# Optimization experiments

Measured on AMD Instinct MI355X. Metric: run time of the kernel, lower is better.

## Reference

```python
import jax, jax.numpy as jnp
import numpy as np
import math

D_MODEL = 128
N_HEAD = 8
D_K = D_MODEL // N_HEAD
NEG_INF = -1e30


def setup_inputs() -> dict:
    key = jax.random.key(0)
    ks = jax.random.split(key, 8)
    B, N, D = 4, 2048, D_MODEL
    s = 1.0 / math.sqrt(D)
    x = jax.random.normal(ks[0], (B, D, N), dtype=jnp.float32)
    mask = jnp.ones((B, N), dtype=jnp.float32)
    Wq = jax.random.normal(ks[1], (D, D), dtype=jnp.float32) * s
    Wk = jax.random.normal(ks[2], (D, D), dtype=jnp.float32) * s
    Wv = jax.random.normal(ks[3], (D, D), dtype=jnp.float32) * s
    Wfc = jax.random.normal(ks[4], (D, D), dtype=jnp.float32) * s
    z = jnp.zeros((D,), dtype=jnp.float32)
    return {"x": x, "mask": mask, "Wq": Wq, "bq": z, "Wk": Wk, "bk": z,
            "Wv": Wv, "bv": z, "Wfc": Wfc, "bfc": z}


def reference(x, mask, Wq, bq, Wk, bk, Wv, bv, Wfc, bfc):
    # x: [B, D, N], mask: [B, N]
    B, D, N = x.shape
    xt = jnp.swapaxes(x, 1, 2)  # [B, N, D]
    q = (xt @ Wq.T + bq).reshape(B, N, N_HEAD, D_K)
    k = (xt @ Wk.T + bk).reshape(B, N, N_HEAD, D_K)
    v = (xt @ Wv.T + bv).reshape(B, N, N_HEAD, D_K)
    # scores: [B, H, Nq, Nk]; NOTE: original scales by sqrt(d_model), not sqrt(d_k)
    scores = jnp.einsum('bnhd,bmhd->bhnm', q, k) / jnp.sqrt(jnp.float32(D))
    # multiplicative mask_logits over the key dimension
    m = mask[:, None, None, :]  # [B, 1, 1, Nk]
    scores = scores * m + (1.0 - m) * NEG_INF
    atten = jax.nn.softmax(scores, axis=-1)  # dropout is identity (p=0 / eval)
    out = jnp.einsum('bhnm,bmhd->bnhd', atten, v).reshape(B, N, D)
    out = out @ Wfc.T + bfc
    return jnp.swapaxes(out, 1, 2)  # [B, D, N]
```

## Files before the change

### kernel.cpp

```cpp
#include <hip/hip_runtime.h>
#include <stdint.h>

#define BSZ  4
#define NSEQ 2048
#define DM   128
#define NH   8
#define DK   16
#define LOG2E 1.4426950408889634f
#define SCALE_QL 0.1275156338341935f
#define W_SCALE 3.814697265625e-6f

typedef __bf16          bf16x8v __attribute__((ext_vector_type(8)));
typedef float           f32x4   __attribute__((ext_vector_type(4)));
typedef float           f32x16  __attribute__((ext_vector_type(16)));
typedef unsigned short  u16x8   __attribute__((ext_vector_type(8)));
typedef unsigned short  u16x4   __attribute__((ext_vector_type(4)));
typedef unsigned int    u32x2   __attribute__((ext_vector_type(2)));
typedef unsigned int    u32x4   __attribute__((ext_vector_type(4)));

__device__ __forceinline__ unsigned short f2bf(float f) {
    unsigned u = __float_as_uint(f);
    u = (u + 0x7fffu + ((u >> 16) & 1u)) >> 16;
    return (unsigned short)u;
}

__device__ __forceinline__ unsigned int pack2bf(float a, float b) {
#if __has_builtin(__builtin_amdgcn_cvt_pk_bf16_f32)
    typedef __bf16 bf16x2 __attribute__((ext_vector_type(2)));
    bf16x2 v = __builtin_amdgcn_cvt_pk_bf16_f32(a, b);
    return __builtin_bit_cast(unsigned int, v);
#else
    return (unsigned)f2bf(a) | ((unsigned)f2bf(b) << 16);
#endif
}

__device__ __forceinline__ float exp2_(float x) {
#if __has_builtin(__builtin_amdgcn_exp2f)
    return __builtin_amdgcn_exp2f(x);
#else
    return exp2f(x);
#endif
}

__device__ __forceinline__ f32x4 mfma16(u16x8 a, u16x8 b, f32x4 c) {
    return __builtin_amdgcn_mfma_f32_16x16x32_bf16(
        __builtin_bit_cast(bf16x8v, a), __builtin_bit_cast(bf16x8v, b), c, 0, 0, 0);
}
__device__ __forceinline__ f32x16 mfma32(u16x8 a, u16x8 b, f32x16 c) {
    return __builtin_amdgcn_mfma_f32_32x32x16_bf16(
        __builtin_bit_cast(bf16x8v, a), __builtin_bit_cast(bf16x8v, b), c, 0, 0, 0);
}

__device__ __forceinline__ void build_bfrags(const f32x16& S, u16x8& bfe, u16x8& bfo) {
    const u32x4 f1 = {pack2bf(S[0],  S[1]),  pack2bf(S[2],  S[3]),
                      pack2bf(S[4],  S[5]),  pack2bf(S[6],  S[7])};
    const u32x4 f2 = {pack2bf(S[8],  S[9]),  pack2bf(S[10], S[11]),
                      pack2bf(S[12], S[13]), pack2bf(S[14], S[15])};
    bfe = __builtin_bit_cast(u16x8, f1);
    bfo = __builtin_bit_cast(u16x8, f2);
}

__global__ __launch_bounds__(256) void k_prep(
    const float* __restrict__ Wq, const float* __restrict__ Wk,
    const float* __restrict__ Wv, const float* __restrict__ Wfc,
    const float* __restrict__ mask,
    unsigned short* __restrict__ WqB, unsigned short* __restrict__ WkB,
    unsigned short* __restrict__ WvB, unsigned short* __restrict__ WfcB,
    unsigned short* __restrict__ VW2)
{
    const int gt = blockIdx.x * 256 + threadIdx.x;
    if (gt < DM * DM) {
        WqB[gt]  = f2bf(Wq[gt] * SCALE_QL);
        WkB[gt]  = f2bf(Wk[gt]);
        WvB[gt]  = f2bf(Wv[gt]);
        WfcB[gt] = f2bf(Wfc[gt]);
    } else if (gt < DM * DM + BSZ * NSEQ) {
        const int i  = gt - DM * DM;
        const int kv = i & (NSEQ - 1);
        const int bb = i >> 11;
        const unsigned short w16 = f2bf(mask[i] * W_SCALE);
        unsigned short* dst = VW2 +
            (((size_t)(bb * NH) * 128 + (kv >> 4)) << 9) +
            (16 + ((kv >> 2) & 1) * 32) * 8 + (kv & 3) + 4 * ((kv >> 3) & 1);
#pragma unroll
        for (int hh = 0; hh < NH; ++hh)
            dst[(size_t)hh * 128 * 512] = w16;
    }
}

__global__ __launch_bounds__(768) void k_qkv(
    const float* __restrict__ x,
    const unsigned short* __restrict__ WqB, const float* __restrict__ bq,
    const unsigned short* __restrict__ WkB, const float* __restrict__ bk,
    const unsigned short* __restrict__ WvB, const float* __restrict__ bv,
    const float* __restrict__ mask,
    unsigned short* __restrict__ Q, unsigned short* __restrict__ Kb,
    unsigned short* __restrict__ VW2)
{
    __shared__ __align__(16) float xs[DM * 36];
    const int tid = threadIdx.x;

    const int b  = blockIdx.x >> 6;
    const int n0 = (blockIdx.x & 63) << 5;

#pragma unroll
    for (int i = tid; i < 1024; i += 768) {
        const int d = i >> 3, c4 = (i & 7) << 2;
        *reinterpret_cast<f32x4*>(&xs[d * 36 + c4]) =
            *reinterpret_cast<const f32x4*>(x + (size_t)(b * DM + d) * NSEQ + n0 + c4);
    }
    __syncthreads();

    const int lane = tid & 63;
    const int wv   = tid >> 6;
    const int mat  = wv >> 2;
    const int nt   = (wv >> 1) & 1;
    const int th   = wv & 1;
    const int c    = lane & 15;
    const int quad = lane >> 4;
    const int col  = n0 + nt * 16 + c;

    u16x8 xf[4];
#pragma unroll
    for (int kk = 0; kk < 4; ++kk) {
        float f[8];
#pragma unroll
        for (int j = 0; j < 8; ++j)
            f[j] = xs[(kk * 32 + quad * 8 + j) * 36 + nt * 16 + c];
        u32x4 u = {pack2bf(f[0], f[1]), pack2bf(f[2], f[3]),
                   pack2bf(f[4], f[5]), pack2bf(f[6], f[7])};
        xf[kk] = __builtin_bit_cast(u16x8, u);
    }

    const unsigned short* W = (mat == 0) ? WqB : (mat == 1) ? WkB : WvB;
    const float* bias = (mat == 0) ? bq : (mat == 1) ? bk : bv;
    const float  sc   = (mat == 0) ? SCALE_QL : 1.0f;
    const float  vwsc = (mat == 2) ? mask[b * NSEQ + col] * W_SCALE : 0.f;
    const int    g    = col >> 4;
    const int    roff = ((col >> 2) & 1) * 32;
    const int    j7   = (col & 3) | (((col >> 3) & 1) << 2);

#pragma unroll
    for (int tt = 0; tt < 4; ++tt) {
        const int t = th * 4 + tt;
        f32x4 acc = {0.f, 0.f, 0.f, 0.f};
#pragma unroll
        for (int kk = 0; kk < 4; ++kk)
            acc = mfma16(*reinterpret_cast<const u16x8*>(
                             W + (t * 16 + c) * DM + kk * 32 + quad * 8),
                         xf[kk], acc);
        if (mat == 2) {
            unsigned short* vwp = VW2 +
                (((size_t)((b * NH + t) * 128 + g)) << 9) + j7;
#pragma unroll
            for (int r = 0; r < 4; ++r)
                vwp[(quad * 4 + r + roff) * 8] =
                    f2bf((acc[r] + bias[t * 16 + quad * 4 + r]) * vwsc);
        } else {
            u16x4 pk;
#pragma unroll
            for (int r = 0; r < 4; ++r)
                pk[r] = f2bf(acc[r] + bias[t * 16 + quad * 4 + r] * sc);
            *reinterpret_cast<u16x4*>(
                (mat == 0 ? Q : Kb) + ((size_t)(b * NH + t) * NSEQ + col) * DK +
                quad * 4) = pk;
        }
    }
}

__global__ __launch_bounds__(256, 4) void k_attn(
    const unsigned short* __restrict__ Q,
    const unsigned short* __restrict__ Kb,
    const unsigned short* __restrict__ VW2,
    unsigned short* __restrict__ AO)
{
    __shared__ __align__(16) float smem[256 + 2 * 4 * 32 * 20];
    const int tid  = threadIdx.x;
    const int lane = tid & 63;
    const int w    = tid >> 6;
    const int q32  = lane & 31;
    const int hi   = lane >> 5;

    const int bid = ((int)blockIdx.x & 7) * 128 + ((int)blockIdx.x >> 3);
    const int b  = bid >> 8;
    const int h  = (bid >> 5) & 7;
    const int n0 = (bid & 31) << 6;
    const int bh = b * NH + h;

    const u16x8 uqA = *reinterpret_cast<const u16x8*>(
        Q + ((size_t)bh * NSEQ + n0 + q32) * DK + 8 * hi);
    const u16x8 uqB = *reinterpret_cast<const u16x8*>(
        Q + ((size_t)bh * NSEQ + n0 + 32 + q32) * DK + 8 * hi);

    const unsigned short* Kp = Kb + (size_t)bh * NSEQ * DK + 8 * hi;
    const unsigned short* Ap = VW2 + (((size_t)bh * 128) << 9) + lane * 8;

    f32x16 accA = {};
    f32x16 accB = {};
    const f32x16 z16 = {};
    const int kvb = w * (NSEQ / 4);

    u16x8 nk0 = *reinterpret_cast<const u16x8*>(Kp + (size_t)(kvb + q32) * DK);
    u16x8 nk1 = *reinterpret_cast<const u16x8*>(Kp + (size_t)(kvb + 32 + q32) * DK);

#pragma unroll 1
    for (int it = 0; it < 8; ++it) {
        const int kv0 = kvb + it * 64;
        const int g0  = kv0 >> 4;
        const u16x8 va0 = *reinterpret_cast<const u16x8*>(Ap + ((size_t)(g0    ) << 9));
        const u16x8 va1 = *reinterpret_cast<const u16x8*>(Ap + ((size_t)(g0 + 1) << 9));
        const u16x8 va2 = *reinterpret_cast<const u16x8*>(Ap + ((size_t)(g0 + 2) << 9));
        const u16x8 va3 = *reinterpret_cast<const u16x8*>(Ap + ((size_t)(g0 + 3) << 9));

        {
            __builtin_amdgcn_s_setprio(1);
            f32x16 SA = mfma32(nk0, uqA, z16);
            f32x16 SB = mfma32(nk0, uqB, z16);
            __builtin_amdgcn_s_setprio(0);
            if (it < 7)
                nk0 = *reinterpret_cast<const u16x8*>(
                    Kp + (size_t)(kv0 + 64 + q32) * DK);
#pragma unroll
            for (int i = 0; i < 16; ++i) SA[i] = exp2_(SA[i]);
#pragma unroll
            for (int i = 0; i < 16; ++i) SB[i] = exp2_(SB[i]);
            u16x8 bfA1, bfA2, bfB1, bfB2;
            build_bfrags(SA, bfA1, bfA2);
            build_bfrags(SB, bfB1, bfB2);
            __builtin_amdgcn_s_setprio(1);
            accA = mfma32(va0, bfA1, accA);
            accB = mfma32(va0, bfB1, accB);
            accA = mfma32(va1, bfA2, accA);
            accB = mfma32(va1, bfB2, accB);
            __builtin_amdgcn_s_setprio(0);
        }

        {
            __builtin_amdgcn_s_setprio(1);
            f32x16 SA = mfma32(nk1, uqA, z16);
            f32x16 SB = mfma32(nk1, uqB, z16);
            __builtin_amdgcn_s_setprio(0);
            if (it < 7)
                nk1 = *reinterpret_cast<const u16x8*>(
                    Kp + (size_t)(kv0 + 96 + q32) * DK);
#pragma unroll
            for (int i = 0; i < 16; ++i) SA[i] = exp2_(SA[i]);
#pragma unroll
            for (int i = 0; i < 16; ++i) SB[i] = exp2_(SB[i]);
            u16x8 bfA1, bfA2, bfB1, bfB2;
            build_bfrags(SA, bfA1, bfA2);
            build_bfrags(SB, bfB1, bfB2);
            __builtin_amdgcn_s_setprio(1);
            accA = mfma32(va2, bfA1, accA);
            accB = mfma32(va2, bfB1, accB);
            accA = mfma32(va3, bfA2, accA);
            accB = mfma32(va3, bfB2, accB);
            __builtin_amdgcn_s_setprio(0);
        }
    }

    float* Lsm = smem;
    float* Osm = smem + 256;
    {
        float* Orow = Osm + w * 640 + q32 * 20;
        *reinterpret_cast<f32x4*>(Orow + (hi ? 4 : 0)) =
            f32x4{accA[0], accA[1], accA[2], accA[3]};
        *reinterpret_cast<f32x4*>(Orow + (hi ? 12 : 8)) =
            f32x4{accA[4], accA[5], accA[6], accA[7]};
        if (!hi) Lsm[w * 32 + q32] = accA[8];
        float* Orow2 = Orow + 2560;
        *reinterpret_cast<f32x4*>(Orow2 + (hi ? 4 : 0)) =
            f32x4{accB[0], accB[1], accB[2], accB[3]};
        *reinterpret_cast<f32x4*>(Orow2 + (hi ? 12 : 8)) =
            f32x4{accB[4], accB[5], accB[6], accB[7]};
        if (!hi) Lsm[128 + w * 32 + q32] = accB[8];
    }
    __syncthreads();

    const int q   = tid >> 3;
    const int dk2 = (tid & 7) * 2;
#pragma unroll
    for (int t2 = 0; t2 < 2; ++t2) {
        const float* Lt = Lsm + t2 * 128;
        const float l = Lt[q] + Lt[32 + q] + Lt[64 + q] + Lt[96 + q];
        const float* Oq = Osm + t2 * 2560 + q * 20 + dk2;
        const float v0 = Oq[0] + Oq[640] + Oq[1280] + Oq[1920];
        const float v1 = Oq[1] + Oq[641] + Oq[1281] + Oq[1921];
        const float inv = 1.0f / l;
        *reinterpret_cast<unsigned int*>(
            AO + ((size_t)(b * NSEQ) + n0 + t2 * 32 + q) * DM + h * DK + dk2) =
            pack2bf(v0 * inv, v1 * inv);
    }
}

__global__ __launch_bounds__(256) void k_fc(
    const unsigned short* __restrict__ AO,
    const unsigned short* __restrict__ WfcB, const float* __restrict__ bfc,
    float* __restrict__ out)
{
    const int lane = threadIdx.x & 63;
    const int w    = threadIdx.x >> 6;
    const int c    = lane & 15;
    const int quad = lane >> 4;
    const int b    = blockIdx.x >> 8;
    const int n0   = ((blockIdx.x >> 1) & 127) << 4;
    const int t    = (blockIdx.x & 1) * 4 + w;

    u16x8 af[4];
#pragma unroll
    for (int kk = 0; kk < 4; ++kk)
        af[kk] = *reinterpret_cast<const u16x8*>(
            AO + ((size_t)(b * NSEQ) + n0 + c) * DM + kk * 32 + quad * 8);

    f32x4 acc = {0.f, 0.f, 0.f, 0.f};
#pragma unroll
    for (int kk = 0; kk < 4; ++kk)
        acc = mfma16(*reinterpret_cast<const u16x8*>(
                         WfcB + (t * 16 + c) * DM + kk * 32 + quad * 8),
                     af[kk], acc);
#pragma unroll
    for (int r = 0; r < 4; ++r)
        out[(size_t)(b * DM + t * 16 + quad * 4 + r) * NSEQ + n0 + c] =
            acc[r] + bfc[t * 16 + quad * 4 + r];
}

extern "C" void kernel_launch(void* const* d_in, const int* in_sizes, int n_in,
                              void* d_out, int out_size, void* d_ws, size_t ws_size,
                              hipStream_t stream)
{
    const float* x    = (const float*)d_in[0];
    const float* mask = (const float*)d_in[1];
    const float* Wq   = (const float*)d_in[2];
    const float* bq   = (const float*)d_in[3];
    const float* Wk   = (const float*)d_in[4];
    const float* bk   = (const float*)d_in[5];
    const float* Wv   = (const float*)d_in[6];
    const float* bv   = (const float*)d_in[7];
    const float* Wfc  = (const float*)d_in[8];
    const float* bfc  = (const float*)d_in[9];
    float* out = (float*)d_out;

    const size_t QKV_ELEMS = (size_t)BSZ * NH * NSEQ * DK;
    unsigned short* Q    = (unsigned short*)d_ws;
    unsigned short* Kb   = Q + QKV_ELEMS;
    unsigned short* AO   = Kb + QKV_ELEMS;
    unsigned short* WfcB = AO + QKV_ELEMS;
    unsigned short* VW2  = WfcB + DM * DM;
    unsigned short* WqB  = VW2 + (size_t)BSZ * NH * 128 * 512;
    unsigned short* WkB  = WqB + DM * DM;
    unsigned short* WvB  = WkB + DM * DM;

    k_prep<<<96, 256, 0, stream>>>(Wq, Wk, Wv, Wfc, mask,
                                   WqB, WkB, WvB, WfcB, VW2);
    k_qkv<<<256, 768, 0, stream>>>(x, WqB, bq, WkB, bk, WvB, bv, mask,
                                   Q, Kb, VW2);
    k_attn<<<1024, 256, 0, stream>>>(Q, Kb, VW2, AO);
    k_fc<<<1024, 256, 0, stream>>>(AO, WfcB, bfc, out);
}
```

Baseline: 116.5 us.

## Software-pipeline QK score MFMAs with PV accumulation across half-iterations

```diff
diff --git a/kernel.cpp b/kernel.cpp
--- a/kernel.cpp
+++ b/kernel.cpp
@@ -51,13 +51,15 @@
         __builtin_bit_cast(bf16x8v, a), __builtin_bit_cast(bf16x8v, b), c, 0, 0, 0);
 }
 
-__device__ __forceinline__ void build_bfrags(const f32x16& S, u16x8& bfe, u16x8& bfo) {
+__device__ __forceinline__ void exppack(f32x16 S, u16x8& b1, u16x8& b2) {
+#pragma unroll
+    for (int i = 0; i < 16; ++i) S[i] = exp2_(S[i]);
     const u32x4 f1 = {pack2bf(S[0],  S[1]),  pack2bf(S[2],  S[3]),
                       pack2bf(S[4],  S[5]),  pack2bf(S[6],  S[7])};
     const u32x4 f2 = {pack2bf(S[8],  S[9]),  pack2bf(S[10], S[11]),
                       pack2bf(S[12], S[13]), pack2bf(S[14], S[15])};
-    bfe = __builtin_bit_cast(u16x8, f1);
-    bfo = __builtin_bit_cast(u16x8, f2);
+    b1 = __builtin_bit_cast(u16x8, f1);
+    b2 = __builtin_bit_cast(u16x8, f2);
 }
 
 __global__ __launch_bounds__(256) void k_prep(
@@ -199,63 +201,71 @@
     f32x16 accB = {};
     const f32x16 z16 = {};
     const int kvb = w * (NSEQ / 4);
-
-    u16x8 nk0 = *reinterpret_cast<const u16x8*>(Kp + (size_t)(kvb + q32) * DK);
-    u16x8 nk1 = *reinterpret_cast<const u16x8*>(Kp + (size_t)(kvb + 32 + q32) * DK);
+    const int gb  = kvb >> 4;
+
+    u16x8 nkE = *reinterpret_cast<const u16x8*>(Kp + (size_t)(kvb + q32) * DK);
+    u16x8 nkO = *reinterpret_cast<const u16x8*>(Kp + (size_t)(kvb + 32 + q32) * DK);
+    u16x8 bfEA1, bfEA2, bfEB1, bfEB2;
+    u16x8 vaE0, vaE1;
+    {
+        __builtin_amdgcn_s_setprio(1);
+        f32x16 SA = mfma32(nkE, uqA, z16);
+        f32x16 SB = mfma32(nkE, uqB, z16);
+        __builtin_amdgcn_s_setprio(0);
+        nkE = *reinterpret_cast<const u16x8*>(Kp + (size_t)(kvb + 64 + q32) * DK);
+        exppack(SA, bfEA1, bfEA2);
+        exppack(SB, bfEB1, bfEB2);
+    }
+    vaE0 = *reinterpret_cast<const u16x8*>(Ap + ((size_t)gb << 9));
+    vaE1 = *reinterpret_cast<const u16x8*>(Ap + ((size_t)(gb + 1) << 9));
 
 #pragma unroll 1
     for (int it = 0; it < 8; ++it) {
-        const int kv0 = kvb + it * 64;
-        const int g0  = kv0 >> 4;
-        const u16x8 va0 = *reinterpret_cast<const u16x8*>(Ap + ((size_t)(g0    ) << 9));
-        const u16x8 va1 = *reinterpret_cast<const u16x8*>(Ap + ((size_t)(g0 + 1) << 9));
-        const u16x8 va2 = *reinterpret_cast<const u16x8*>(Ap + ((size_t)(g0 + 2) << 9));
-        const u16x8 va3 = *reinterpret_cast<const u16x8*>(Ap + ((size_t)(g0 + 3) << 9));
-
+        const int kvs = kvb + it * 64;
+        const int g0  = gb + it * 4;
+
+        u16x8 bfOA1, bfOA2, bfOB1, bfOB2, vaO0, vaO1;
         {
             __builtin_amdgcn_s_setprio(1);
-            f32x16 SA = mfma32(nk0, uqA, z16);
-            f32x16 SB = mfma32(nk0, uqB, z16);
+            f32x16 SA = mfma32(nkO, uqA, z16);
+            accA = mfma32(vaE0, bfEA1, accA);
+            accB = mfma32(vaE0, bfEB1, accB);
+            accA = mfma32(vaE1, bfEA2, accA);
+            accB = mfma32(vaE1, bfEB2, accB);
+            __builtin_amdgcn_s_setprio(0);
+            exppack(SA, bfOA1, bfOA2);
+            __builtin_amdgcn_s_setprio(1);
+            f32x16 SB = mfma32(nkO, uqB, z16);
             __builtin_amdgcn_s_setprio(0);
             if (it < 7)
-                nk0 = *reinterpret_cast<const u16x8*>(
-                    Kp + (size_t)(kv0 + 64 + q32) * DK);
-#pragma unroll
-            for (int i = 0; i < 16; ++i) SA[i] = exp2_(SA[i]);
-#pragma unroll
-            for (int i = 0; i < 16; ++i) SB[i] = exp2_(SB[i]);
-            u16x8 bfA1, bfA2, bfB1, bfB2;
-            build_bfrags(SA, bfA1, bfA2);
-            build_bfrags(SB, bfB1, bfB2);
-            __builtin_amdgcn_s_setprio(1);
-            accA = mfma32(va0, bfA1, accA);
-            accB = mfma32(va0, bfB1, accB);
-            accA = mfma32(va1, bfA2, accA);
-            accB = mfma32(va1, bfB2, accB);
-            __builtin_amdgcn_s_setprio(0);
+                nkO = *reinterpret_cast<const u16x8*>(
+                    Kp + (size_t)(kvs + 96 + q32) * DK);
+            exppack(SB, bfOB1, bfOB2);
+            vaO0 = *reinterpret_cast<const u16x8*>(Ap + ((size_t)(g0 + 2) << 9));
+            vaO1 = *reinterpret_cast<const u16x8*>(Ap + ((size_t)(g0 + 3) << 9));
         }
 
         {
             __builtin_amdgcn_s_setprio(1);
-            f32x16 SA = mfma32(nk1, uqA, z16);
-            f32x16 SB = mfma32(nk1, uqB, z16);
+            f32x16 SA;
+            if (it < 7) SA = mfma32(nkE, uqA, z16);
+            accA = mfma32(vaO0, bfOA1, accA);
+            accB = mfma32(vaO0, bfOB1, accB);
+            accA = mfma32(vaO1, bfOA2, accA);
+            accB = mfma32(vaO1, bfOB2, accB);
             __builtin_amdgcn_s_setprio(0);
-            if (it < 7)
-                nk1 = *reinterpret_cast<const u16x8*>(
-                    Kp + (size_t)(kv0 + 96 + q32) * DK);
-#pragma unroll
-            for (int i = 0; i < 16; ++i) SA[i] = exp2_(SA[i]);
-#pragma unroll
-            for (int i = 0; i < 16; ++i) SB[i] = exp2_(SB[i]);
-            u16x8 bfA1, bfA2, bfB1, bfB2;
-            build_bfrags(SA, bfA1, bfA2);
-            build_bfrags(SB, bfB1, bfB2);
-            __builtin_amdgcn_s_setprio(1);
-            accA = mfma32(va2, bfA1, accA);
-            accB = mfma32(va2, bfB1, accB);
-            accA = mfma32(va3, bfA2, accA);
-            accB = mfma32(va3, bfB2, accB);
-            __builtin_amdgcn_s_setprio(0);
+            if (it < 7) {
+                exppack(SA, bfEA1, bfEA2);
+                __builtin_amdgcn_s_setprio(1);
+                f32x16 SB = mfma32(nkE, uqB, z16);
+                __builtin_amdgcn_s_setprio(0);
+                if (it < 6)
+                    nkE = *reinterpret_cast<const u16x8*>(
+                        Kp + (size_t)(kvs + 128 + q32) * DK);
+                exppack(SB, bfEB1, bfEB2);
+                vaE0 = *reinterpret_cast<const u16x8*>(Ap + ((size_t)(g0 + 4) << 9));
+                vaE1 = *reinterpret_cast<const u16x8*>(Ap + ((size_t)(g0 + 5) << 9));
+            }
         }
     }
 
```

Measured after the change: 126.6 us. 1.09x slower.
